# Kernel tuning notes

Hardware: AMD Instinct MI355X
Metric: run time of the kernel (lower is better)

## Reference

```python
import jax, jax.numpy as jnp
from jax import lax
import numpy as np

NUM_TAGS = 17
B, S = 2048, 512


def setup_inputs() -> dict:
    key = jax.random.key(0)
    k1, k2, k3, k4, k5 = jax.random.split(key, 5)
    inputs = jax.random.normal(k1, (B, S, NUM_TAGS), dtype=jnp.float32)
    tags = jax.random.randint(k2, (B, S), 0, NUM_TAGS, dtype=jnp.int64)
    mask = jnp.ones((B, S), dtype=jnp.int32)
    # learned CRF parameters (xavier-ish / normal init like the torch module)
    transitions = jax.random.normal(k3, (NUM_TAGS, NUM_TAGS), dtype=jnp.float32) * (2.0 / NUM_TAGS) ** 0.5
    start_transitions = jax.random.normal(k4, (NUM_TAGS,), dtype=jnp.float32)
    end_transitions = jax.random.normal(k5, (NUM_TAGS,), dtype=jnp.float32)
    return {"inputs": inputs, "tags": tags, "mask": mask,
            "transitions": transitions,
            "start_transitions": start_transitions,
            "end_transitions": end_transitions}


def _crf_loss(inputs, tags, mask, transitions, start_transitions, end_transitions):
    b, s, t = inputs.shape
    maskf = mask.astype(inputs.dtype)  # (B,S)

    # ---- log partition (denominator): sequential forward recurrence ----
    alpha0 = inputs[:, 0] + start_transitions[None, :]  # (B,T)

    def step(alpha, xm):
        logit_t, m_t = xm  # (B,T), (B,)
        # inner[b,i,j] = alpha[b,i] + emit[b,j] + trans[i,j]
        inner = alpha[:, :, None] + logit_t[:, None, :] + transitions[None, :, :]
        new_alpha = jax.nn.logsumexp(inner, axis=1)  # (B,T)
        alpha = new_alpha * m_t[:, None] + alpha * (1.0 - m_t)[:, None]
        return alpha, None

    xs = (jnp.swapaxes(inputs, 0, 1)[1:], jnp.swapaxes(maskf, 0, 1)[1:])  # (S-1,B,T),(S-1,B)
    alpha, _ = lax.scan(step, alpha0, xs)
    log_denominator = jax.nn.logsumexp(alpha + end_transitions[None, :], axis=-1)  # (B,)

    # ---- gold path score (numerator), fully vectorized over time ----
    score = start_transitions[tags[:, 0]]  # (B,)
    trans_sc = transitions[tags[:, :-1], tags[:, 1:]]  # (B,S-1)
    emit_sc = jnp.take_along_axis(inputs[:, :-1], tags[:, :-1, None], axis=2)[..., 0]  # (B,S-1)
    score = score + jnp.sum(trans_sc * maskf[:, 1:] + emit_sc * maskf[:, :-1], axis=1)
    last_idx = jnp.sum(mask, axis=1).astype(jnp.int32) - 1  # (B,)
    last_tags = jnp.take_along_axis(tags, last_idx[:, None].astype(tags.dtype), axis=1)[:, 0]
    last_input = jnp.take_along_axis(inputs[:, -1], last_tags[:, None], axis=1)[:, 0]
    score = score + end_transitions[last_tags] + last_input * maskf[:, -1]

    return jnp.sum(score - log_denominator)


def reference(inputs, tags, mask, transitions, start_transitions, end_transitions):
    return _crf_loss(inputs, tags, mask, transitions, start_transitions, end_transitions)
```

## Files before the change

kernel.cpp:

```cpp
#include <hip/hip_runtime.h>

#define B_ 2048
#define S_ 512
#define T_ 17
#define RECN 256
#define FWDW 448
#define MAINW 896

typedef float v16f __attribute__((ext_vector_type(16)));
typedef short v8s  __attribute__((ext_vector_type(8)));
typedef float f4u  __attribute__((ext_vector_type(4), aligned(4)));

union frag_u { unsigned u[4]; v8s v; };

static __device__ inline unsigned pkbf(float lo, float hi) {
    unsigned r;
    asm("v_cvt_pk_bf16_f32 %0, %1, %2" : "=v"(r) : "v"(lo), "v"(hi));
    return r;
}

#define PACKB(S0,S1,S2,S3,S4,S5,S6,S7, BOUT) do {                            \
    unsigned P0_ = pkbf(S0, S1), P1_ = pkbf(S2, S3);                         \
    unsigned R0_ = pkbf(S4, S5), R1_ = pkbf(S6, S7);                         \
    auto s0_ = __builtin_amdgcn_permlane32_swap(P0_, R0_, false, false);     \
    auto s1_ = __builtin_amdgcn_permlane32_swap(P1_, R1_, false, false);     \
    BOUT.u[0] = s0_[0]; BOUT.u[1] = s1_[0];                                  \
    BOUT.u[2] = s0_[1]; BOUT.u[3] = s1_[1];                                  \
} while (0)

#define W16SWAP() do {                                                       \
    auto rw_ = __builtin_amdgcn_permlane32_swap(__float_as_uint(W8),         \
                                                __float_as_uint(W8),         \
                                                false, false);               \
    w16 = __uint_as_float(rw_[0]);                                           \
} while (0)

#define LOADK8(Q0, Q1, SS, MA, MB, T0_) do {                                 \
    const float* bp_ = ip + (size_t)(T0_) * T_;                              \
    _Pragma("unroll") for (int u_ = 0; u_ < 8; ++u_) {                       \
        Q0[u_] = *(const f4u*)(bp_ + u_ * T_ + 4 * h);                       \
        Q1[u_] = *(const f4u*)(bp_ + u_ * T_ + 8 + 4 * h);                   \
        SS[u_] = bp_[u_ * T_ + 16];                                          \
    }                                                                        \
    MA = *(const int4*)(mp + (T0_));                                         \
    MB = *(const int4*)(mp + (T0_) + 4);                                     \
} while (0)

#define FSTEP(Q0u, Q1u, Su, Mu) do {                                         \
    frag_u Bf_;                                                              \
    PACKB(W0,W1,W2,W3,W4,W5,W6,W7, Bf_);                                     \
    v16f acc_ = __builtin_amdgcn_mfma_f32_32x32x16_bf16(A1.v, Bf_.v, zacc,0,0,0); \
    float d0_=__expf((Q0u).x), d1_=__expf((Q0u).y);                          \
    float d2_=__expf((Q0u).z), d3_=__expf((Q0u).w);                          \
    float d4_=__expf((Q1u).x), d5_=__expf((Q1u).y);                          \
    float d6_=__expf((Q1u).z), d7_=__expf((Q1u).w);                          \
    float d8_=__expf(Su);                                                    \
    bool bm_ = (Mu) != 0;                                                    \
    float n0_ = fmaf(E16[0], w16, acc_[0]) * d0_;                            \
    float n1_ = fmaf(E16[1], w16, acc_[1]) * d1_;                            \
    float n2_ = fmaf(E16[2], w16, acc_[2]) * d2_;                            \
    float n3_ = fmaf(E16[3], w16, acc_[3]) * d3_;                            \
    float n4_ = fmaf(E16[4], w16, acc_[4]) * d4_;                            \
    float n5_ = fmaf(E16[5], w16, acc_[5]) * d5_;                            \
    float n6_ = fmaf(E16[6], w16, acc_[6]) * d6_;                            \
    float n7_ = fmaf(E16[7], w16, acc_[7]) * d7_;                            \
    float n8_ = fmaf(E16[8], w16, acc_[8]) * d8_;                            \
    W0=bm_?n0_:W0; W1=bm_?n1_:W1; W2=bm_?n2_:W2; W3=bm_?n3_:W3;              \
    W4=bm_?n4_:W4; W5=bm_?n5_:W5; W6=bm_?n6_:W6; W7=bm_?n7_:W7;              \
    W8=bm_?n8_:W8;                                                           \
    W16SWAP();                                                               \
} while (0)

#define BSTEP(Q0u, Q1u, Su, Mu) do {                                         \
    float d0_=__expf((Q0u).x), d1_=__expf((Q0u).y);                          \
    float d2_=__expf((Q0u).z), d3_=__expf((Q0u).w);                          \
    float d4_=__expf((Q1u).x), d5_=__expf((Q1u).y);                          \
    float d6_=__expf((Q1u).z), d7_=__expf((Q1u).w);                          \
    float d8_=__expf(Su);                                                    \
    float U16_ = w16 * d8_;                                                  \
    frag_u Bf_;                                                              \
    PACKB(W0*d0_, W1*d1_, W2*d2_, W3*d3_,                                    \
          W4*d4_, W5*d5_, W6*d6_, W7*d7_, Bf_);                              \
    v16f acc_ = __builtin_amdgcn_mfma_f32_32x32x16_bf16(A1.v, Bf_.v, zacc,0,0,0); \
    bool bm_ = (Mu) != 0;                                                    \
    float n0_ = fmaf(E16[0], U16_, acc_[0]);                                 \
    float n1_ = fmaf(E16[1], U16_, acc_[1]);                                 \
    float n2_ = fmaf(E16[2], U16_, acc_[2]);                                 \
    float n3_ = fmaf(E16[3], U16_, acc_[3]);                                 \
    float n4_ = fmaf(E16[4], U16_, acc_[4]);                                 \
    float n5_ = fmaf(E16[5], U16_, acc_[5]);                                 \
    float n6_ = fmaf(E16[6], U16_, acc_[6]);                                 \
    float n7_ = fmaf(E16[7], U16_, acc_[7]);                                 \
    float n8_ = fmaf(E16[8], U16_, acc_[8]);                                 \
    W0=bm_?n0_:W0; W1=bm_?n1_:W1; W2=bm_?n2_:W2; W3=bm_?n3_:W3;              \
    W4=bm_?n4_:W4; W5=bm_?n5_:W5; W6=bm_?n6_:W6; W7=bm_?n7_:W7;              \
    W8=bm_?n8_:W8;                                                           \
    W16SWAP();                                                               \
} while (0)

#define RENORM() do {                                                        \
    float M_ = fmaxf(fmaxf(fmaxf(W0,W1),fmaxf(W2,W3)),                       \
                     fmaxf(fmaxf(W4,W5),fmaxf(fmaxf(W6,W7),W8)));            \
    auto rm_ = __builtin_amdgcn_permlane32_swap(__float_as_uint(M_),         \
                                                __float_as_uint(M_),         \
                                                false, false);               \
    M_ = fmaxf(__uint_as_float(rm_[0]), __uint_as_float(rm_[1]));            \
    float r_ = 1.0f / M_;                                                    \
    Z += __logf(M_);                                                         \
    W0*=r_; W1*=r_; W2*=r_; W3*=r_; W4*=r_;                                  \
    W5*=r_; W6*=r_; W7*=r_; W8*=r_; w16*=r_;                                 \
} while (0)

#define FCH8(Q0a, Q1a, Sa, Ma, Mb) do {                                      \
    FSTEP(Q0a[0], Q1a[0], Sa[0], (Ma).x);                                    \
    FSTEP(Q0a[1], Q1a[1], Sa[1], (Ma).y);                                    \
    FSTEP(Q0a[2], Q1a[2], Sa[2], (Ma).z);                                    \
    FSTEP(Q0a[3], Q1a[3], Sa[3], (Ma).w);                                    \
    RENORM();                                                                \
    FSTEP(Q0a[4], Q1a[4], Sa[4], (Mb).x);                                    \
    FSTEP(Q0a[5], Q1a[5], Sa[5], (Mb).y);                                    \
    FSTEP(Q0a[6], Q1a[6], Sa[6], (Mb).z);                                    \
    FSTEP(Q0a[7], Q1a[7], Sa[7], (Mb).w);                                    \
    RENORM();                                                                \
} while (0)

#define BCH8(Q0a, Q1a, Sa, Ma, Mb) do {                                      \
    BSTEP(Q0a[7], Q1a[7], Sa[7], (Mb).w);                                    \
    BSTEP(Q0a[6], Q1a[6], Sa[6], (Mb).z);                                    \
    BSTEP(Q0a[5], Q1a[5], Sa[5], (Mb).y);                                    \
    BSTEP(Q0a[4], Q1a[4], Sa[4], (Mb).x);                                    \
    RENORM();                                                                \
    BSTEP(Q0a[3], Q1a[3], Sa[3], (Ma).w);                                    \
    BSTEP(Q0a[2], Q1a[2], Sa[2], (Ma).z);                                    \
    BSTEP(Q0a[1], Q1a[1], Sa[1], (Ma).y);                                    \
    BSTEP(Q0a[0], Q1a[0], Sa[0], (Ma).x);                                    \
    RENORM();                                                                \
} while (0)

static __device__ void helper_score(int s, int lane,
                                    const int* __restrict__ tags,
                                    const int* __restrict__ mask,
                                    const float* __restrict__ inputs,
                                    const float* __restrict__ startt,
                                    const float* __restrict__ endt,
                                    const float* tl, float* recs)
{
    const int* tp = tags + (size_t)s * S_;
    const int* mp = mask + (size_t)s * S_;
    const float* ib = inputs + (size_t)s * (S_ * T_);
    const int4* tp4 = (const int4*)tp;
    const int4* mp4 = (const int4*)mp;

    int4 t0 = tp4[2 * lane], t1 = tp4[2 * lane + 1];
    int4 m0 = mp4[2 * lane], m1 = mp4[2 * lane + 1];
    int tg[8] = {t0.x, t0.y, t0.z, t0.w, t1.x, t1.y, t1.z, t1.w};
    int mi[8] = {m0.x, m0.y, m0.z, m0.w, m1.x, m1.y, m1.z, m1.w};
    int tprev = (lane > 0) ? tp[8 * lane - 1] : 0;

    float e = 0.0f, tr = 0.0f;
    int ms = 0;
#pragma unroll
    for (int u = 0; u < 8; ++u) {
        int t = 8 * lane + u;
        float mf = (float)mi[u];
        float gate = (t <= S_ - 2) ? mf : 0.0f;
        e = fmaf(gate, ib[(size_t)t * T_ + tg[u]], e);
        int pt = (u == 0) ? tprev : tg[u - 1];
        float tv = tl[pt * T_ + tg[u]];
        tr = fmaf((t >= 1) ? mf : 0.0f, tv, tr);
        ms += mi[u];
    }
    for (int d = 1; d < 64; d <<= 1) {
        e  += __shfl_xor(e, d);
        tr += __shfl_xor(tr, d);
        ms += __shfl_xor(ms, d);
    }
    if (lane == 0) {
        int li = ms - 1; if (li < 0) li = 0;
        int lt = tp[li];
        float ml = (float)mp[S_ - 1];
        float lin = ib[(size_t)(S_ - 1) * T_ + lt];
        float sc = startt[tp[0]] + tr + e + endt[lt] + lin * ml;
        recs[(size_t)s * RECN + 252] = sc;
    }
}

__global__ __launch_bounds__(64) void crf_seg(
    const float* __restrict__ inputs, const int* __restrict__ tags,
    const int* __restrict__ mask, const float* __restrict__ trans,
    const float* __restrict__ startt, const float* __restrict__ endt,
    float* __restrict__ ws)
{
    __shared__ float tl[T_ * T_];
    const int lane = (int)threadIdx.x;
    const int bid = (int)blockIdx.x;
    for (int k = lane; k < T_ * T_; k += 64) tl[k] = trans[k];
    __syncthreads();

    if (bid < MAINW) {
        const bool isF = (bid < FWDW);
        const int widx = isF ? bid : bid - FWDW;
        const int j = widx >> 6;
        const int sg = widx & 63;
        const int h = lane >> 5;
        const int col = lane & 31;
        const int seq = sg * 32 + col;

        frag_u A1;
#pragma unroll
        for (int wd = 0; wd < 4; ++wd) {
            const int k0 = 8 * h + 2 * wd, k1 = k0 + 1;
            float e0 = 0.0f, e1 = 0.0f;
            if (col < 17) {
                e0 = isF ? __expf(tl[k0 * T_ + col]) : __expf(tl[col * T_ + k0]);
                e1 = isF ? __expf(tl[k1 * T_ + col]) : __expf(tl[col * T_ + k1]);
            }
            A1.u[wd] = pkbf(e0, e1);
        }
        float E16[9];
#pragma unroll
        for (int k = 0; k < 4; ++k) {
            const int r0 = 4 * h + k, r1 = 8 + 4 * h + k;
            E16[k]     = __expf(isF ? tl[16 * T_ + r0] : tl[r0 * T_ + 16]);
            E16[4 + k] = __expf(isF ? tl[16 * T_ + r1] : tl[r1 * T_ + 16]);
        }
        E16[8] = (h == 0) ? __expf(tl[16 * T_ + 16]) : 0.0f;

        v16f zacc;
#pragma unroll
        for (int r = 0; r < 16; ++r) zacc[r] = 0.0f;

        const float* ip = inputs + (size_t)seq * (S_ * T_);
        const int*   mp = mask + (size_t)seq * S_;

        float W0, W1, W2, W3, W4, W5, W6, W7, W8, w16, Z = 0.0f;
        f4u X0[8], X1[8]; float XS[8]; int4 XM0, XM1;
        f4u Y0[8], Y1[8]; float YS[8]; int4 YM0, YM1;

        int off;
        if (isF) {
            if (j == 0) {
                LOADK8(X0, X1, XS, XM0, XM1, 0);
                LOADK8(Y0, Y1, YS, YM0, YM1, 8);
                f4u s0 = *(const f4u*)(startt + 4 * h);
                f4u s1 = *(const f4u*)(startt + 8 + 4 * h);
                W0 = __expf(X0[0].x + s0.x); W1 = __expf(X0[0].y + s0.y);
                W2 = __expf(X0[0].z + s0.z); W3 = __expf(X0[0].w + s0.w);
                W4 = __expf(X1[0].x + s1.x); W5 = __expf(X1[0].y + s1.y);
                W6 = __expf(X1[0].z + s1.z); W7 = __expf(X1[0].w + s1.w);
                W8 = h ? 0.0f : __expf(XS[0] + startt[16]);
                W16SWAP();
                FSTEP(X0[1], X1[1], XS[1], XM0.y);
                FSTEP(X0[2], X1[2], XS[2], XM0.z);
                FSTEP(X0[3], X1[3], XS[3], XM0.w);
                RENORM();
                FSTEP(X0[4], X1[4], XS[4], XM1.x);
                FSTEP(X0[5], X1[5], XS[5], XM1.y);
                FSTEP(X0[6], X1[6], XS[6], XM1.z);
                FSTEP(X0[7], X1[7], XS[7], XM1.w);
                RENORM();
                for (int c = 0; c < 3; ++c) {
                    LOADK8(X0, X1, XS, XM0, XM1, 16 + 16 * c);
                    FCH8(Y0, Y1, YS, YM0, YM1);
                    LOADK8(Y0, Y1, YS, YM0, YM1, 24 + 16 * c);
                    FCH8(X0, X1, XS, XM0, XM1);
                }
                FCH8(Y0, Y1, YS, YM0, YM1);
            } else {
                const int tb = 64 * j;
                LOADK8(X0, X1, XS, XM0, XM1, tb);
                LOADK8(Y0, Y1, YS, YM0, YM1, tb + 8);
                W0=W1=W2=W3=W4=W5=W6=W7 = 1.0f;
                W8 = h ? 0.0f : 1.0f;
                W16SWAP();
                for (int c = 0; c < 3; ++c) {
                    FCH8(X0, X1, XS, XM0, XM1);
                    LOADK8(X0, X1, XS, XM0, XM1, tb + 16 + 16 * c);
                    FCH8(Y0, Y1, YS, YM0, YM1);
                    LOADK8(Y0, Y1, YS, YM0, YM1, tb + 24 + 16 * c);
                }
                FCH8(X0, X1, XS, XM0, XM1);
                FCH8(Y0, Y1, YS, YM0, YM1);
            }
            off = j * 18;
        } else {
            const int jb = j + 1;
            const int tb = 64 * jb;
            LOADK8(X0, X1, XS, XM0, XM1, tb + 56);
            LOADK8(Y0, Y1, YS, YM0, YM1, tb + 48);
            if (jb == 7) {
                f4u e0 = *(const f4u*)(endt + 4 * h);
                f4u e1 = *(const f4u*)(endt + 8 + 4 * h);
                W0 = __expf(e0.x); W1 = __expf(e0.y);
                W2 = __expf(e0.z); W3 = __expf(e0.w);
                W4 = __expf(e1.x); W5 = __expf(e1.y);
                W6 = __expf(e1.z); W7 = __expf(e1.w);
                W8 = h ? 0.0f : __expf(endt[16]);
            } else {
                W0=W1=W2=W3=W4=W5=W6=W7 = 1.0f;
                W8 = h ? 0.0f : 1.0f;
            }
            W16SWAP();
            for (int c = 0; c < 3; ++c) {
                BCH8(X0, X1, XS, XM0, XM1);
                LOADK8(X0, X1, XS, XM0, XM1, tb + 40 - 16 * c);
                BCH8(Y0, Y1, YS, YM0, YM1);
                LOADK8(Y0, Y1, YS, YM0, YM1, tb + 32 - 16 * c);
            }
            BCH8(X0, X1, XS, XM0, XM1);
            BCH8(Y0, Y1, YS, YM0, YM1);
            off = 126 + (jb - 1) * 18;
        }

        float* rec = ws + (size_t)seq * RECN + off;
        rec[4*h+0] = W0; rec[4*h+1] = W1; rec[4*h+2] = W2; rec[4*h+3] = W3;
        rec[8+4*h+0] = W4; rec[8+4*h+1] = W5; rec[8+4*h+2] = W6; rec[8+4*h+3] = W7;
        if (h == 0) { rec[16] = W8; rec[17] = Z; }
    } else {
        helper_score(bid - MAINW, lane, tags, mask, inputs, startt, endt, tl, ws);
    }
}

__global__ __launch_bounds__(256) void crf_comb(const float* __restrict__ recs,
                                                float* __restrict__ partial)
{
    __shared__ float sm[256];
    const int tid = (int)threadIdx.x;
    const int s = (int)blockIdx.x * 256 + tid;

    float a = 0.0f;
    {
        const float* r = recs + (size_t)s * RECN;
        float zsum = r[17];
        float logn = 0.0f;
#pragma unroll
        for (int j = 1; j <= 7; ++j) {
            const float* G = r + 126 + (j - 1) * 18;
            const float* F = r + (j - 1) * 18;
            float dot = 0.0f;
#pragma unroll
            for (int i = 0; i < T_; ++i) dot = fmaf(G[i], F[i], dot);
            logn += __logf(dot);
            zsum += G[17];
        }
#pragma unroll
        for (int j = 1; j <= 6; ++j) {
            const float* F = r + j * 18;
            float sf = 0.0f;
#pragma unroll
            for (int i = 0; i < T_; ++i) sf += F[i];
            logn -= __logf(sf);
        }
        a = r[252] - (logn + zsum);
    }
    sm[tid] = a;
    __syncthreads();
    for (int k = 128; k >= 1; k >>= 1) {
        if (tid < k) sm[tid] += sm[tid + k];
        __syncthreads();
    }
    if (tid == 0) partial[blockIdx.x] = sm[0];
}

__global__ __launch_bounds__(64) void crf_red(const float* __restrict__ partial,
                                              float* __restrict__ out)
{
    if (threadIdx.x == 0) {
        float s = 0.0f;
#pragma unroll
        for (int i = 0; i < 8; ++i) s += partial[i];
        out[0] = s;
    }
}

extern "C" void kernel_launch(void* const* d_in, const int* in_sizes, int n_in,
                              void* d_out, int out_size, void* d_ws, size_t ws_size,
                              hipStream_t stream)
{
    const float* inputs = (const float*)d_in[0];
    const int*   tags   = (const int*)d_in[1];
    const int*   mask   = (const int*)d_in[2];
    const float* trans  = (const float*)d_in[3];
    const float* startt = (const float*)d_in[4];
    const float* endt   = (const float*)d_in[5];
    float* out = (float*)d_out;
    float* ws  = (float*)d_ws;
    float* partial = ws + (size_t)B_ * RECN;

    crf_seg<<<MAINW + B_, 64, 0, stream>>>(inputs, tags, mask, trans,
                                           startt, endt, ws);
    crf_comb<<<B_ / 256, 256, 0, stream>>>(ws, partial);
    crf_red<<<1, 64, 0, stream>>>(partial, out);
}
```

Before: 55.78 us.

## Fuse gold-path score into forward/backward segment waves, drop helper blocks

```diff
diff --git a/kernel.cpp b/kernel.cpp
--- a/kernel.cpp
+++ b/kernel.cpp
@@ -3,7 +3,7 @@
 #define B_ 2048
 #define S_ 512
 #define T_ 17
-#define RECN 256
+#define RECN 288
 #define FWDW 448
 #define MAINW 896
 
@@ -35,7 +35,7 @@
     w16 = __uint_as_float(rw_[0]);                                           \
 } while (0)
 
-#define LOADK8(Q0, Q1, SS, MA, MB, T0_) do {                                 \
+#define LOADK8(Q0, Q1, SS, MA, MB, TGa, TPM1, T0_) do {                      \
     const float* bp_ = ip + (size_t)(T0_) * T_;                              \
     _Pragma("unroll") for (int u_ = 0; u_ < 8; ++u_) {                       \
         Q0[u_] = *(const f4u*)(bp_ + u_ * T_ + 4 * h);                       \
@@ -44,6 +44,37 @@
     }                                                                        \
     MA = *(const int4*)(mp + (T0_));                                         \
     MB = *(const int4*)(mp + (T0_) + 4);                                     \
+    { int4 ta_ = *(const int4*)(tp + (T0_));                                 \
+      int4 tb_ = *(const int4*)(tp + (T0_) + 4);                             \
+      TGa[0]=ta_.x; TGa[1]=ta_.y; TGa[2]=ta_.z; TGa[3]=ta_.w;                \
+      TGa[4]=tb_.x; TGa[5]=tb_.y; TGa[6]=tb_.z; TGa[7]=tb_.w; }              \
+    TPM1 = tp[(T0_) > 0 ? (T0_) - 1 : 0];                                    \
+} while (0)
+
+#define SCORE8(Q0a, Q1a, Sa, TGa, MA, MB, TPM1, T0_) do {                    \
+    if (own) {                                                               \
+        int pt_ = (TPM1);                                                    \
+        int mv_[8] = {(MA).x,(MA).y,(MA).z,(MA).w,                           \
+                      (MB).x,(MB).y,(MB).z,(MB).w};                          \
+        _Pragma("unroll") for (int u_ = 0; u_ < 8; ++u_) {                   \
+            const int t_ = (T0_) + u_;                                       \
+            const int tg_ = TGa[u_];                                         \
+            const float mf_ = (float)mv_[u_];                                \
+            f4u q0_ = Q0a[u_], q1_ = Q1a[u_];                                \
+            float ev_ = (tg_==4*h+0)?q0_.x:(tg_==4*h+1)?q0_.y:               \
+                        (tg_==4*h+2)?q0_.z:(tg_==4*h+3)?q0_.w:               \
+                        (tg_==8+4*h+0)?q1_.x:(tg_==8+4*h+1)?q1_.y:           \
+                        (tg_==8+4*h+2)?q1_.z:(tg_==8+4*h+3)?q1_.w:           \
+                        ((h==0)&&(tg_==16))?Sa[u_]:0.0f;                     \
+            acc_e = fmaf((t_ <= S_-2)?mf_:0.0f, ev_, acc_e);                 \
+            if (h == 0) {                                                    \
+                float tv_ = tl[pt_*T_ + tg_];                                \
+                acc_tr = fmaf((t_>=1)?mf_:0.0f, tv_, acc_tr);                \
+                msum += mv_[u_];                                             \
+            }                                                                \
+            pt_ = tg_;                                                       \
+        }                                                                    \
+    }                                                                        \
 } while (0)
 
 #define FSTEP(Q0u, Q1u, Su, Mu) do {                                         \
@@ -137,54 +168,6 @@
     RENORM();                                                                \
 } while (0)
 
-static __device__ void helper_score(int s, int lane,
-                                    const int* __restrict__ tags,
-                                    const int* __restrict__ mask,
-                                    const float* __restrict__ inputs,
-                                    const float* __restrict__ startt,
-                                    const float* __restrict__ endt,
-                                    const float* tl, float* recs)
-{
-    const int* tp = tags + (size_t)s * S_;
-    const int* mp = mask + (size_t)s * S_;
-    const float* ib = inputs + (size_t)s * (S_ * T_);
-    const int4* tp4 = (const int4*)tp;
-    const int4* mp4 = (const int4*)mp;
-
-    int4 t0 = tp4[2 * lane], t1 = tp4[2 * lane + 1];
-    int4 m0 = mp4[2 * lane], m1 = mp4[2 * lane + 1];
-    int tg[8] = {t0.x, t0.y, t0.z, t0.w, t1.x, t1.y, t1.z, t1.w};
-    int mi[8] = {m0.x, m0.y, m0.z, m0.w, m1.x, m1.y, m1.z, m1.w};
-    int tprev = (lane > 0) ? tp[8 * lane - 1] : 0;
-
-    float e = 0.0f, tr = 0.0f;
-    int ms = 0;
-#pragma unroll
-    for (int u = 0; u < 8; ++u) {
-        int t = 8 * lane + u;
-        float mf = (float)mi[u];
-        float gate = (t <= S_ - 2) ? mf : 0.0f;
-        e = fmaf(gate, ib[(size_t)t * T_ + tg[u]], e);
-        int pt = (u == 0) ? tprev : tg[u - 1];
-        float tv = tl[pt * T_ + tg[u]];
-        tr = fmaf((t >= 1) ? mf : 0.0f, tv, tr);
-        ms += mi[u];
-    }
-    for (int d = 1; d < 64; d <<= 1) {
-        e  += __shfl_xor(e, d);
-        tr += __shfl_xor(tr, d);
-        ms += __shfl_xor(ms, d);
-    }
-    if (lane == 0) {
-        int li = ms - 1; if (li < 0) li = 0;
-        int lt = tp[li];
-        float ml = (float)mp[S_ - 1];
-        float lin = ib[(size_t)(S_ - 1) * T_ + lt];
-        float sc = startt[tp[0]] + tr + e + endt[lt] + lin * ml;
-        recs[(size_t)s * RECN + 252] = sc;
-    }
-}
-
 __global__ __launch_bounds__(64) void crf_seg(
     const float* __restrict__ inputs, const int* __restrict__ tags,
     const int* __restrict__ mask, const float* __restrict__ trans,
@@ -197,132 +180,159 @@
     for (int k = lane; k < T_ * T_; k += 64) tl[k] = trans[k];
     __syncthreads();
 
-    if (bid < MAINW) {
-        const bool isF = (bid < FWDW);
-        const int widx = isF ? bid : bid - FWDW;
-        const int j = widx >> 6;
-        const int sg = widx & 63;
-        const int h = lane >> 5;
-        const int col = lane & 31;
-        const int seq = sg * 32 + col;
-
-        frag_u A1;
-#pragma unroll
-        for (int wd = 0; wd < 4; ++wd) {
-            const int k0 = 8 * h + 2 * wd, k1 = k0 + 1;
-            float e0 = 0.0f, e1 = 0.0f;
-            if (col < 17) {
-                e0 = isF ? __expf(tl[k0 * T_ + col]) : __expf(tl[col * T_ + k0]);
-                e1 = isF ? __expf(tl[k1 * T_ + col]) : __expf(tl[col * T_ + k1]);
+    const bool isF = (bid < FWDW);
+    const int widx = isF ? bid : bid - FWDW;
+    const int j = widx >> 6;
+    const int sg = widx & 63;
+    const int h = lane >> 5;
+    const int col = lane & 31;
+    const int seq = sg * 32 + col;
+    const int jb = j + 1;
+    const bool own = isF ? (j <= 3) : (jb >= 4);
+
+    frag_u A1;
+#pragma unroll
+    for (int wd = 0; wd < 4; ++wd) {
+        const int k0 = 8 * h + 2 * wd, k1 = k0 + 1;
+        float e0 = 0.0f, e1 = 0.0f;
+        if (col < 17) {
+            e0 = isF ? __expf(tl[k0 * T_ + col]) : __expf(tl[col * T_ + k0]);
+            e1 = isF ? __expf(tl[k1 * T_ + col]) : __expf(tl[col * T_ + k1]);
+        }
+        A1.u[wd] = pkbf(e0, e1);
+    }
+    float E16[9];
+#pragma unroll
+    for (int k = 0; k < 4; ++k) {
+        const int r0 = 4 * h + k, r1 = 8 + 4 * h + k;
+        E16[k]     = __expf(isF ? tl[16 * T_ + r0] : tl[r0 * T_ + 16]);
+        E16[4 + k] = __expf(isF ? tl[16 * T_ + r1] : tl[r1 * T_ + 16]);
+    }
+    E16[8] = (h == 0) ? __expf(tl[16 * T_ + 16]) : 0.0f;
+
+    v16f zacc;
+#pragma unroll
+    for (int r = 0; r < 16; ++r) zacc[r] = 0.0f;
+
+    const float* ip = inputs + (size_t)seq * (S_ * T_);
+    const int*   mp = mask + (size_t)seq * S_;
+    const int*   tp = tags + (size_t)seq * S_;
+
+    float W0, W1, W2, W3, W4, W5, W6, W7, W8, w16, Z = 0.0f;
+    float acc_e = 0.0f, acc_tr = 0.0f;
+    int msum = 0;
+    f4u X0[8], X1[8]; float XS[8]; int4 XM0, XM1; int XT[8]; int XTP;
+    f4u Y0[8], Y1[8]; float YS[8]; int4 YM0, YM1; int YT[8]; int YTP;
+
+    int off;
+    if (isF) {
+        if (j == 0) {
+            LOADK8(X0, X1, XS, XM0, XM1, XT, XTP, 0);
+            LOADK8(Y0, Y1, YS, YM0, YM1, YT, YTP, 8);
+            f4u s0 = *(const f4u*)(startt + 4 * h);
+            f4u s1 = *(const f4u*)(startt + 8 + 4 * h);
+            W0 = __expf(X0[0].x + s0.x); W1 = __expf(X0[0].y + s0.y);
+            W2 = __expf(X0[0].z + s0.z); W3 = __expf(X0[0].w + s0.w);
+            W4 = __expf(X1[0].x + s1.x); W5 = __expf(X1[0].y + s1.y);
+            W6 = __expf(X1[0].z + s1.z); W7 = __expf(X1[0].w + s1.w);
+            W8 = h ? 0.0f : __expf(XS[0] + startt[16]);
+            W16SWAP();
+            FSTEP(X0[1], X1[1], XS[1], XM0.y);
+            FSTEP(X0[2], X1[2], XS[2], XM0.z);
+            FSTEP(X0[3], X1[3], XS[3], XM0.w);
+            RENORM();
+            FSTEP(X0[4], X1[4], XS[4], XM1.x);
+            FSTEP(X0[5], X1[5], XS[5], XM1.y);
+            FSTEP(X0[6], X1[6], XS[6], XM1.z);
+            FSTEP(X0[7], X1[7], XS[7], XM1.w);
+            RENORM();
+            SCORE8(X0, X1, XS, XT, XM0, XM1, XTP, 0);
+            for (int c = 0; c < 3; ++c) {
+                LOADK8(X0, X1, XS, XM0, XM1, XT, XTP, 16 + 16 * c);
+                FCH8(Y0, Y1, YS, YM0, YM1);
+                SCORE8(Y0, Y1, YS, YT, YM0, YM1, YTP, 8 + 16 * c);
+                LOADK8(Y0, Y1, YS, YM0, YM1, YT, YTP, 24 + 16 * c);
+                FCH8(X0, X1, XS, XM0, XM1);
+                SCORE8(X0, X1, XS, XT, XM0, XM1, XTP, 16 + 16 * c);
             }
-            A1.u[wd] = pkbf(e0, e1);
-        }
-        float E16[9];
-#pragma unroll
-        for (int k = 0; k < 4; ++k) {
-            const int r0 = 4 * h + k, r1 = 8 + 4 * h + k;
-            E16[k]     = __expf(isF ? tl[16 * T_ + r0] : tl[r0 * T_ + 16]);
-            E16[4 + k] = __expf(isF ? tl[16 * T_ + r1] : tl[r1 * T_ + 16]);
-        }
-        E16[8] = (h == 0) ? __expf(tl[16 * T_ + 16]) : 0.0f;
-
-        v16f zacc;
-#pragma unroll
-        for (int r = 0; r < 16; ++r) zacc[r] = 0.0f;
-
-        const float* ip = inputs + (size_t)seq * (S_ * T_);
-        const int*   mp = mask + (size_t)seq * S_;
-
-        float W0, W1, W2, W3, W4, W5, W6, W7, W8, w16, Z = 0.0f;
-        f4u X0[8], X1[8]; float XS[8]; int4 XM0, XM1;
-        f4u Y0[8], Y1[8]; float YS[8]; int4 YM0, YM1;
-
-        int off;
-        if (isF) {
-            if (j == 0) {
-                LOADK8(X0, X1, XS, XM0, XM1, 0);
-                LOADK8(Y0, Y1, YS, YM0, YM1, 8);
-                f4u s0 = *(const f4u*)(startt + 4 * h);
-                f4u s1 = *(const f4u*)(startt + 8 + 4 * h);
-                W0 = __expf(X0[0].x + s0.x); W1 = __expf(X0[0].y + s0.y);
-                W2 = __expf(X0[0].z + s0.z); W3 = __expf(X0[0].w + s0.w);
-                W4 = __expf(X1[0].x + s1.x); W5 = __expf(X1[0].y + s1.y);
-                W6 = __expf(X1[0].z + s1.z); W7 = __expf(X1[0].w + s1.w);
-                W8 = h ? 0.0f : __expf(XS[0] + startt[16]);
-                W16SWAP();
-                FSTEP(X0[1], X1[1], XS[1], XM0.y);
-                FSTEP(X0[2], X1[2], XS[2], XM0.z);
-                FSTEP(X0[3], X1[3], XS[3], XM0.w);
-                RENORM();
-                FSTEP(X0[4], X1[4], XS[4], XM1.x);
-                FSTEP(X0[5], X1[5], XS[5], XM1.y);
-                FSTEP(X0[6], X1[6], XS[6], XM1.z);
-                FSTEP(X0[7], X1[7], XS[7], XM1.w);
-                RENORM();
-                for (int c = 0; c < 3; ++c) {
-                    LOADK8(X0, X1, XS, XM0, XM1, 16 + 16 * c);
-                    FCH8(Y0, Y1, YS, YM0, YM1);
-                    LOADK8(Y0, Y1, YS, YM0, YM1, 24 + 16 * c);
-                    FCH8(X0, X1, XS, XM0, XM1);
-                }
-                FCH8(Y0, Y1, YS, YM0, YM1);
-            } else {
-                const int tb = 64 * j;
-                LOADK8(X0, X1, XS, XM0, XM1, tb);
-                LOADK8(Y0, Y1, YS, YM0, YM1, tb + 8);
-                W0=W1=W2=W3=W4=W5=W6=W7 = 1.0f;
-                W8 = h ? 0.0f : 1.0f;
-                W16SWAP();
-                for (int c = 0; c < 3; ++c) {
-                    FCH8(X0, X1, XS, XM0, XM1);
-                    LOADK8(X0, X1, XS, XM0, XM1, tb + 16 + 16 * c);
-                    FCH8(Y0, Y1, YS, YM0, YM1);
-                    LOADK8(Y0, Y1, YS, YM0, YM1, tb + 24 + 16 * c);
-                }
-                FCH8(X0, X1, XS, XM0, XM1);
-                FCH8(Y0, Y1, YS, YM0, YM1);
-            }
-            off = j * 18;
+            FCH8(Y0, Y1, YS, YM0, YM1);
+            SCORE8(Y0, Y1, YS, YT, YM0, YM1, YTP, 56);
         } else {
-            const int jb = j + 1;
-            const int tb = 64 * jb;
-            LOADK8(X0, X1, XS, XM0, XM1, tb + 56);
-            LOADK8(Y0, Y1, YS, YM0, YM1, tb + 48);
-            if (jb == 7) {
-                f4u e0 = *(const f4u*)(endt + 4 * h);
-                f4u e1 = *(const f4u*)(endt + 8 + 4 * h);
-                W0 = __expf(e0.x); W1 = __expf(e0.y);
-                W2 = __expf(e0.z); W3 = __expf(e0.w);
-                W4 = __expf(e1.x); W5 = __expf(e1.y);
-                W6 = __expf(e1.z); W7 = __expf(e1.w);
-                W8 = h ? 0.0f : __expf(endt[16]);
-            } else {
-                W0=W1=W2=W3=W4=W5=W6=W7 = 1.0f;
-                W8 = h ? 0.0f : 1.0f;
-            }
+            const int tb = 64 * j;
+            LOADK8(X0, X1, XS, XM0, XM1, XT, XTP, tb);
+            LOADK8(Y0, Y1, YS, YM0, YM1, YT, YTP, tb + 8);
+            W0=W1=W2=W3=W4=W5=W6=W7 = 1.0f;
+            W8 = h ? 0.0f : 1.0f;
             W16SWAP();
             for (int c = 0; c < 3; ++c) {
-                BCH8(X0, X1, XS, XM0, XM1);
-                LOADK8(X0, X1, XS, XM0, XM1, tb + 40 - 16 * c);
-                BCH8(Y0, Y1, YS, YM0, YM1);
-                LOADK8(Y0, Y1, YS, YM0, YM1, tb + 32 - 16 * c);
+                FCH8(X0, X1, XS, XM0, XM1);
+                SCORE8(X0, X1, XS, XT, XM0, XM1, XTP, tb + 16 * c);
+                LOADK8(X0, X1, XS, XM0, XM1, XT, XTP, tb + 16 + 16 * c);
+                FCH8(Y0, Y1, YS, YM0, YM1);
+                SCORE8(Y0, Y1, YS, YT, YM0, YM1, YTP, tb + 8 + 16 * c);
+                LOADK8(Y0, Y1, YS, YM0, YM1, YT, YTP, tb + 24 + 16 * c);
             }
+            FCH8(X0, X1, XS, XM0, XM1);
+            SCORE8(X0, X1, XS, XT, XM0, XM1, XTP, tb + 48);
+            FCH8(Y0, Y1, YS, YM0, YM1);
+            SCORE8(Y0, Y1, YS, YT, YM0, YM1, YTP, tb + 56);
+        }
+        off = j * 18;
+    } else {
+        const int tb = 64 * jb;
+        LOADK8(X0, X1, XS, XM0, XM1, XT, XTP, tb + 56);
+        LOADK8(Y0, Y1, YS, YM0, YM1, YT, YTP, tb + 48);
+        if (jb == 7) {
+            f4u e0 = *(const f4u*)(endt + 4 * h);
+            f4u e1 = *(const f4u*)(endt + 8 + 4 * h);
+            W0 = __expf(e0.x); W1 = __expf(e0.y);
+            W2 = __expf(e0.z); W3 = __expf(e0.w);
+            W4 = __expf(e1.x); W5 = __expf(e1.y);
+            W6 = __expf(e1.z); W7 = __expf(e1.w);
+            W8 = h ? 0.0f : __expf(endt[16]);
+        } else {
+            W0=W1=W2=W3=W4=W5=W6=W7 = 1.0f;
+            W8 = h ? 0.0f : 1.0f;
+        }
+        W16SWAP();
+        for (int c = 0; c < 3; ++c) {
             BCH8(X0, X1, XS, XM0, XM1);
+            SCORE8(X0, X1, XS, XT, XM0, XM1, XTP, tb + 56 - 16 * c);
+            LOADK8(X0, X1, XS, XM0, XM1, XT, XTP, tb + 40 - 16 * c);
             BCH8(Y0, Y1, YS, YM0, YM1);
-            off = 126 + (jb - 1) * 18;
-        }
-
-        float* rec = ws + (size_t)seq * RECN + off;
-        rec[4*h+0] = W0; rec[4*h+1] = W1; rec[4*h+2] = W2; rec[4*h+3] = W3;
-        rec[8+4*h+0] = W4; rec[8+4*h+1] = W5; rec[8+4*h+2] = W6; rec[8+4*h+3] = W7;
-        if (h == 0) { rec[16] = W8; rec[17] = Z; }
-    } else {
-        helper_score(bid - MAINW, lane, tags, mask, inputs, startt, endt, tl, ws);
+            SCORE8(Y0, Y1, YS, YT, YM0, YM1, YTP, tb + 48 - 16 * c);
+            LOADK8(Y0, Y1, YS, YM0, YM1, YT, YTP, tb + 32 - 16 * c);
+        }
+        BCH8(X0, X1, XS, XM0, XM1);
+        SCORE8(X0, X1, XS, XT, XM0, XM1, XTP, tb + 8);
+        BCH8(Y0, Y1, YS, YM0, YM1);
+        SCORE8(Y0, Y1, YS, YT, YM0, YM1, YTP, tb + 0);
+        off = 126 + (jb - 1) * 18;
+    }
+
+    float* rec = ws + (size_t)seq * RECN + off;
+    rec[4*h+0] = W0; rec[4*h+1] = W1; rec[4*h+2] = W2; rec[4*h+3] = W3;
+    rec[8+4*h+0] = W4; rec[8+4*h+1] = W5; rec[8+4*h+2] = W6; rec[8+4*h+3] = W7;
+    if (h == 0) { rec[16] = W8; rec[17] = Z; }
+
+    if (own) {
+        auto re_ = __builtin_amdgcn_permlane32_swap(__float_as_uint(acc_e),
+                                                    __float_as_uint(acc_e),
+                                                    false, false);
+        float etot = acc_e + __uint_as_float(re_[1]);
+        if (h == 0) {
+            const int soff = isF ? (252 + 3 * j) : (264 + 3 * (jb - 4));
+            float* sr = ws + (size_t)seq * RECN + soff;
+            sr[0] = etot; sr[1] = acc_tr; sr[2] = (float)msum;
+        }
     }
 }
 
-__global__ __launch_bounds__(256) void crf_comb(const float* __restrict__ recs,
-                                                float* __restrict__ partial)
+__global__ __launch_bounds__(256) void crf_comb(
+    const float* __restrict__ recs, const float* __restrict__ inputs,
+    const int* __restrict__ tags, const int* __restrict__ mask,
+    const float* __restrict__ startt, const float* __restrict__ endt,
+    float* __restrict__ partial)
 {
     __shared__ float sm[256];
     const int tid = (int)threadIdx.x;
@@ -351,7 +361,20 @@
             for (int i = 0; i < T_; ++i) sf += F[i];
             logn -= __logf(sf);
         }
-        a = r[252] - (logn + zsum);
+        float e = 0.0f, tr = 0.0f, msf = 0.0f;
+#pragma unroll
+        for (int k = 0; k < 8; ++k) {
+            e   += r[252 + 3 * k];
+            tr  += r[253 + 3 * k];
+            msf += r[254 + 3 * k];
+        }
+        int ms = (int)(msf + 0.5f);
+        int li = ms - 1; if (li < 0) li = 0;
+        int lt = tags[(size_t)s * S_ + li];
+        float ml = (float)mask[(size_t)s * S_ + (S_ - 1)];
+        float lin = inputs[((size_t)s * S_ + (S_ - 1)) * T_ + lt];
+        float sc = startt[tags[(size_t)s * S_]] + tr + e + endt[lt] + lin * ml;
+        a = sc - (logn + zsum);
     }
     sm[tid] = a;
     __syncthreads();
@@ -387,8 +410,9 @@
     float* ws  = (float*)d_ws;
     float* partial = ws + (size_t)B_ * RECN;
 
-    crf_seg<<<MAINW + B_, 64, 0, stream>>>(inputs, tags, mask, trans,
-                                           startt, endt, ws);
-    crf_comb<<<B_ / 256, 256, 0, stream>>>(ws, partial);
+    crf_seg<<<MAINW, 64, 0, stream>>>(inputs, tags, mask, trans,
+                                      startt, endt, ws);
+    crf_comb<<<B_ / 256, 256, 0, stream>>>(ws, inputs, tags, mask,
+                                           startt, endt, partial);
     crf_red<<<1, 64, 0, stream>>>(partial, out);
 }
```

Result: slower. 76.89 us (+37.8%).
